# Kernel optimization log

Hardware: AMD Instinct MI355X
Metric: run time of the kernel (lower is better)

Reference implementation:

```python
import jax, jax.numpy as jnp
import numpy as np

DIM = 768
HEADS = 12
HEAD_DIM = DIM // HEADS
HIDDEN = int(DIM * 4.0)
EPS = 1e-5


def _layernorm(x, g, b):
    mu = jnp.mean(x, axis=-1, keepdims=True)
    var = jnp.var(x, axis=-1, keepdims=True)
    return (x - mu) * jax.lax.rsqrt(var + EPS) * g + b


def setup_inputs() -> dict:
    key = jax.random.key(0)
    ks = jax.random.split(key, 12)
    s = 0.02
    return {
        "x": jax.random.normal(ks[0], (8, 1024, DIM), dtype=jnp.float32),
        "norm1_g": jnp.ones((DIM,), jnp.float32),
        "norm1_b": jnp.zeros((DIM,), jnp.float32),
        "qkv_w": jax.random.normal(ks[1], (3 * DIM, DIM), jnp.float32) * s,
        "qkv_b": jnp.zeros((3 * DIM,), jnp.float32),
        "proj_w": jax.random.normal(ks[2], (DIM, DIM), jnp.float32) * s,
        "proj_b": jnp.zeros((DIM,), jnp.float32),
        "norm2_g": jnp.ones((DIM,), jnp.float32),
        "norm2_b": jnp.zeros((DIM,), jnp.float32),
        "fc1_w": jax.random.normal(ks[3], (HIDDEN, DIM), jnp.float32) * s,
        "fc1_b": jnp.zeros((HIDDEN,), jnp.float32),
        "fc2_w": jax.random.normal(ks[4], (DIM, HIDDEN), jnp.float32) * s,
        "fc2_b": jnp.zeros((DIM,), jnp.float32),
    }


def reference(x, norm1_g, norm1_b, qkv_w, qkv_b, proj_w, proj_b,
              norm2_g, norm2_b, fc1_w, fc1_b, fc2_w, fc2_b):
    B, N, C = x.shape
    scale = HEAD_DIM ** -0.5

    # --- MHSA with pre-norm + residual ---
    h = _layernorm(x, norm1_g, norm1_b)
    qkv = h @ qkv_w.T + qkv_b                      # [B, N, 3C]
    qkv = qkv.reshape(B, N, 3, HEADS, HEAD_DIM)
    qkv = jnp.transpose(qkv, (2, 0, 3, 1, 4))      # [3, B, H, N, Dh]
    q, k, v = qkv[0], qkv[1], qkv[2]
    attn = jnp.einsum("bhnd,bhmd->bhnm", q, k) * scale
    attn = jax.nn.softmax(attn, axis=-1)
    o = jnp.einsum("bhnm,bhmd->bhnd", attn, v)     # [B, H, N, Dh]
    o = jnp.transpose(o, (0, 2, 1, 3)).reshape(B, N, C)
    x = x + (o @ proj_w.T + proj_b)

    # --- MLP with pre-norm + residual ---
    h = _layernorm(x, norm2_g, norm2_b)
    h = jax.nn.gelu(h @ fc1_w.T + fc1_b, approximate=False)
    x = x + (h @ fc2_w.T + fc2_b)
    return x
```

## Files before the change

### kernel.cpp

```cpp
#include <hip/hip_runtime.h>
#include <hip/hip_bf16.h>

typedef unsigned short u16;
using short8  = __attribute__((ext_vector_type(8))) short;
using floatx4 = __attribute__((ext_vector_type(4))) float;

__device__ inline u16 f2bu(float f) {
    __hip_bfloat16 h = __float2bfloat16(f);
    return __builtin_bit_cast(u16, h);
}
__device__ inline float b2f(u16 u) {
    unsigned v = (unsigned)u << 16;
    return __builtin_bit_cast(float, v);
}
__device__ inline float gelu_f(float v) {
    float u = 1.5957691216f * (v + 0.044715f * v * v * v);
    return v / (1.f + __expf(-u));
}

__device__ inline void load16(const u16* g, u16* l) {
    __builtin_amdgcn_global_load_lds(
        (const __attribute__((address_space(1))) void*)g,
        (__attribute__((address_space(3))) void*)l, 16, 0, 0);
}

__global__ void cvt_bf16v(const float4* __restrict__ in, ushort4* __restrict__ out, int n4) {
    int i = blockIdx.x * 256 + threadIdx.x;
    if (i < n4) {
        float4 f = in[i];
        ushort4 r;
        r.x = f2bu(f.x); r.y = f2bu(f.y); r.z = f2bu(f.z); r.w = f2bu(f.w);
        out[i] = r;
    }
}

__global__ __launch_bounds__(256) void layernorm_bf16(
    const float* __restrict__ x, const float* __restrict__ g,
    const float* __restrict__ b, u16* __restrict__ out)
{
    int row = blockIdx.x;
    int tid = threadIdx.x;
    const float* xr = x + (size_t)row * 768;
    float v0 = xr[tid], v1 = xr[tid + 256], v2 = xr[tid + 512];
    float s = v0 + v1 + v2;
    float ss = v0 * v0 + v1 * v1 + v2 * v2;
    for (int off = 1; off < 64; off <<= 1) {
        s  += __shfl_xor(s, off, 64);
        ss += __shfl_xor(ss, off, 64);
    }
    __shared__ float as[4], ass[4];
    int wave = tid >> 6, lane = tid & 63;
    if (lane == 0) { as[wave] = s; ass[wave] = ss; }
    __syncthreads();
    s  = as[0] + as[1] + as[2] + as[3];
    ss = ass[0] + ass[1] + ass[2] + ass[3];
    float mu  = s * (1.0f / 768.0f);
    float var = ss * (1.0f / 768.0f) - mu * mu;
    float rs  = rsqrtf(var + 1e-5f);
    u16* orow = out + (size_t)row * 768;
    orow[tid]       = f2bu((v0 - mu) * rs * g[tid]       + b[tid]);
    orow[tid + 256] = f2bu((v1 - mu) * rs * g[tid + 256] + b[tid + 256]);
    orow[tid + 512] = f2bu((v2 - mu) * rs * g[tid + 512] + b[tid + 512]);
}

__global__ __launch_bounds__(256) void red2(
    const ushort4* __restrict__ P0, const ushort4* __restrict__ P1,
    const float* __restrict__ bias, const float4* __restrict__ res,
    float4* __restrict__ out)
{
    int i = blockIdx.x * 256 + threadIdx.x;
    int col = (i % 192) * 4;
    ushort4 a = P0[i], b = P1[i];
    float4 o = res ? res[i] : out[i];
    o.x += bias[col + 0] + b2f(a.x) + b2f(b.x);
    o.y += bias[col + 1] + b2f(a.y) + b2f(b.y);
    o.z += bias[col + 2] + b2f(a.z) + b2f(b.z);
    o.w += bias[col + 3] + b2f(a.w) + b2f(b.w);
    out[i] = o;
}

__global__ __launch_bounds__(256) void gemm_k64(
    const u16* __restrict__ A, int lda,
    const u16* __restrict__ B, int ldb,
    int K,
    const float* __restrict__ bias,
    const float* __restrict__ res,
    float* __restrict__ outf, u16* __restrict__ outb,
    u16* __restrict__ parts, size_t pstride,
    int ldc, int act, int splits)
{
    __shared__ u16 lsa[128 * 64];
    __shared__ u16 lsb[128 * 64];

    int tid  = threadIdx.x;
    int wave = tid >> 6, lane = tid & 63;
    int quad = lane >> 4, l16 = lane & 15;
    int wrow = (wave >> 1) * 64;
    int wcol = (wave & 1) * 64;

    int gx = gridDim.x;
    int nblk = gx * gridDim.y;
    int flat = blockIdx.y * gx + blockIdx.x;
    int d = (flat & 7) * (nblk >> 3) + (flat >> 3);
    int m0 = (d / gx) * 128, n0 = (d % gx) * 128;

    int Kper = K / splits;
    int kbeg = blockIdx.z * Kper;

    floatx4 acc[4][4];
    for (int i = 0; i < 4; ++i)
        for (int j = 0; j < 4; ++j)
            acc[i][j] = (floatx4){0.f, 0.f, 0.f, 0.f};

    int rsub = lane >> 3;
    int gc   = (lane & 7) ^ rsub;
    const u16* gA[4];
    const u16* gB[4];
    #pragma unroll
    for (int j = 0; j < 4; ++j) {
        int r = (j * 4 + wave) * 8 + rsub;
        gA[j] = A + (size_t)(m0 + r) * lda + kbeg + gc * 8;
        gB[j] = B + (size_t)(n0 + r) * ldb + kbeg + gc * 8;
    }

    int xq0 = ((quad)     ^ (l16 & 7)) * 8;
    int xq1 = ((quad + 4) ^ (l16 & 7)) * 8;

    for (int k0 = 0; k0 < Kper; k0 += 64) {
        __syncthreads();
        #pragma unroll
        for (int j = 0; j < 4; ++j) {
            load16(gA[j], &lsa[(j * 4 + wave) * 512]);
            gA[j] += 64;
        }
        #pragma unroll
        for (int j = 0; j < 4; ++j) {
            load16(gB[j], &lsb[(j * 4 + wave) * 512]);
            gB[j] += 64;
        }
        __syncthreads();

        short8 af[4], bfr[4];
        #pragma unroll
        for (int rb = 0; rb < 4; ++rb) af[rb]  = *(short8*)&lsa[(wrow + rb * 16 + l16) * 64 + xq0];
        #pragma unroll
        for (int cb = 0; cb < 4; ++cb) bfr[cb] = *(short8*)&lsb[(wcol + cb * 16 + l16) * 64 + xq0];
        #pragma unroll
        for (int rb = 0; rb < 4; ++rb)
            #pragma unroll
            for (int cb = 0; cb < 4; ++cb)
                acc[rb][cb] = __builtin_amdgcn_mfma_f32_16x16x32_bf16(af[rb], bfr[cb], acc[rb][cb], 0, 0, 0);
        #pragma unroll
        for (int rb = 0; rb < 4; ++rb) af[rb]  = *(short8*)&lsa[(wrow + rb * 16 + l16) * 64 + xq1];
        #pragma unroll
        for (int cb = 0; cb < 4; ++cb) bfr[cb] = *(short8*)&lsb[(wcol + cb * 16 + l16) * 64 + xq1];
        #pragma unroll
        for (int rb = 0; rb < 4; ++rb)
            #pragma unroll
            for (int cb = 0; cb < 4; ++cb)
                acc[rb][cb] = __builtin_amdgcn_mfma_f32_16x16x32_bf16(af[rb], bfr[cb], acc[rb][cb], 0, 0, 0);
    }

    u16* pdst = (splits > 1) ? parts + (size_t)blockIdx.z * pstride : nullptr;
    #pragma unroll
    for (int rb = 0; rb < 4; ++rb)
        #pragma unroll
        for (int cb = 0; cb < 4; ++cb)
            #pragma unroll
            for (int r = 0; r < 4; ++r) {
                int row = m0 + wrow + rb * 16 + quad * 4 + r;
                int col = n0 + wcol + cb * 16 + l16;
                float v = acc[rb][cb][r];
                if (splits > 1) {
                    pdst[(size_t)row * ldc + col] = f2bu(v);
                } else {
                    v += bias[col];
                    if (res) v += res[(size_t)row * ldc + col];
                    if (act) v = gelu_f(v);
                    if (outf) outf[(size_t)row * ldc + col] = v;
                    else      outb[(size_t)row * ldc + col] = f2bu(v);
                }
            }
}

__global__ __launch_bounds__(256) void attn_fused(
    const u16* __restrict__ qkv, u16* __restrict__ o)
{
    const int N = 1024, C3 = 2304;
    int qb = blockIdx.x;
    int bh = blockIdx.y;
    int b = bh / 12, h = bh % 12;
    int tid = threadIdx.x, wave = tid >> 6, lane = tid & 63;
    int quad = lane >> 4, l16 = lane & 15;

    __shared__ u16 lk[64 * 64];
    __shared__ u16 lvt[64][72];
    __shared__ u16 lp[4][16][72];

    const size_t base = (size_t)b * N * C3;
    int q0 = qb * 64 + wave * 16;

    short8 qa0 = *(const short8*)&qkv[base + (size_t)(q0 + l16) * C3 + h * 64 + quad * 8];
    short8 qa1 = *(const short8*)&qkv[base + (size_t)(q0 + l16) * C3 + h * 64 + 32 + quad * 8];

    floatx4 oacc[4];
    for (int i = 0; i < 4; ++i) oacc[i] = (floatx4){0.f, 0.f, 0.f, 0.f};
    float lsum[4] = {0.f, 0.f, 0.f, 0.f};

    for (int kt = 0; kt < N; kt += 64) {
        __syncthreads();
        #pragma unroll
        for (int i = 0; i < 2; ++i) {
            int idx = i * 2048 + wave * 512 + lane * 8;
            int r = idx >> 6;
            int gc = (lane & 7) ^ (r & 7);
            load16(&qkv[base + (size_t)(kt + r) * C3 + 768 + h * 64 + gc * 8], &lk[idx]);
        }
        {
            int key = tid & 63, dbase = (tid >> 6) * 16;
            const u16* vp = &qkv[base + (size_t)(kt + key) * C3 + 1536 + h * 64 + dbase];
            uint4 vv0 = *(const uint4*)vp;
            uint4 vv1 = *(const uint4*)(vp + 8);
            const u16* e0 = (const u16*)&vv0;
            const u16* e1 = (const u16*)&vv1;
            #pragma unroll
            for (int i = 0; i < 8; ++i) {
                lvt[dbase + i][key]     = e0[i];
                lvt[dbase + 8 + i][key] = e1[i];
            }
        }
        __syncthreads();

        float p[4][4];
        #pragma unroll
        for (int kb = 0; kb < 4; ++kb) {
            int R = kb * 16 + l16;
            short8 b0 = *(short8*)&lk[R * 64 + ((quad ^ (R & 7)) * 8)];
            short8 b1 = *(short8*)&lk[R * 64 + (((quad + 4) ^ (R & 7)) * 8)];
            floatx4 c = (floatx4){0.f, 0.f, 0.f, 0.f};
            c = __builtin_amdgcn_mfma_f32_16x16x32_bf16(qa0, b0, c, 0, 0, 0);
            c = __builtin_amdgcn_mfma_f32_16x16x32_bf16(qa1, b1, c, 0, 0, 0);
            #pragma unroll
            for (int r = 0; r < 4; ++r) {
                p[kb][r] = __expf(c[r] * 0.125f);
                lsum[r] += p[kb][r];
            }
        }
        #pragma unroll
        for (int kb = 0; kb < 4; ++kb)
            #pragma unroll
            for (int r = 0; r < 4; ++r)
                lp[wave][quad * 4 + r][kb * 16 + l16] = f2bu(p[kb][r]);

        short8 pa0 = *(short8*)&lp[wave][l16][quad * 8];
        short8 pa1 = *(short8*)&lp[wave][l16][32 + quad * 8];
        #pragma unroll
        for (int db = 0; db < 4; ++db) {
            short8 vb0 = *(short8*)&lvt[db * 16 + l16][quad * 8];
            short8 vb1 = *(short8*)&lvt[db * 16 + l16][32 + quad * 8];
            oacc[db] = __builtin_amdgcn_mfma_f32_16x16x32_bf16(pa0, vb0, oacc[db], 0, 0, 0);
            oacc[db] = __builtin_amdgcn_mfma_f32_16x16x32_bf16(pa1, vb1, oacc[db], 0, 0, 0);
        }
    }

    #pragma unroll
    for (int r = 0; r < 4; ++r)
        for (int off = 1; off < 16; off <<= 1)
            lsum[r] += __shfl_xor(lsum[r], off, 64);

    #pragma unroll
    for (int db = 0; db < 4; ++db)
        #pragma unroll
        for (int r = 0; r < 4; ++r) {
            int row = q0 + quad * 4 + r;
            int col = h * 64 + db * 16 + l16;
            o[(size_t)(b * N + row) * 768 + col] = f2bu(oacc[db][r] / lsum[r]);
        }
}

extern "C" void kernel_launch(void* const* d_in, const int* in_sizes, int n_in,
                              void* d_out, int out_size, void* d_ws, size_t ws_size,
                              hipStream_t stream) {
    const float* x      = (const float*)d_in[0];
    const float* n1g    = (const float*)d_in[1];
    const float* n1b    = (const float*)d_in[2];
    const float* qkv_w  = (const float*)d_in[3];
    const float* qkv_b  = (const float*)d_in[4];
    const float* proj_w = (const float*)d_in[5];
    const float* proj_b = (const float*)d_in[6];
    const float* n2g    = (const float*)d_in[7];
    const float* n2b    = (const float*)d_in[8];
    const float* fc1_w  = (const float*)d_in[9];
    const float* fc1_b  = (const float*)d_in[10];
    const float* fc2_w  = (const float*)d_in[11];
    const float* fc2_b  = (const float*)d_in[12];
    float* out = (float*)d_out;

    const int T = 8192;
    char* ws = (char*)d_ws;
    u16* w_qkv  = (u16*)ws;               ws += (size_t)2304 * 768 * 2;
    u16* w_proj = (u16*)ws;               ws += (size_t)768 * 768 * 2;
    u16* w_fc1  = (u16*)ws;               ws += (size_t)3072 * 768 * 2;
    u16* w_fc2  = (u16*)ws;               ws += (size_t)768 * 3072 * 2;
    u16* h_buf  = (u16*)ws;               ws += (size_t)T * 768 * 2;
    u16* qkvbuf = (u16*)ws;               ws += (size_t)T * 2304 * 2;
    u16* o_buf  = (u16*)ws;               ws += (size_t)T * 768 * 2;
    u16* pbuf   = (u16*)ws;               ws += (size_t)T * 768 * 2;
    u16* fc1out = qkvbuf;
    bool do_split = (size_t)(ws - (char*)d_ws) <= ws_size;
    size_t pstr = (size_t)(pbuf - h_buf);

    cvt_bf16v<<<dim3(2304 * 768 / 4 / 256), 256, 0, stream>>>((const float4*)qkv_w,  (ushort4*)w_qkv,  2304 * 768 / 4);
    cvt_bf16v<<<dim3(768 * 768 / 4 / 256),  256, 0, stream>>>((const float4*)proj_w, (ushort4*)w_proj, 768 * 768 / 4);
    cvt_bf16v<<<dim3(3072 * 768 / 4 / 256), 256, 0, stream>>>((const float4*)fc1_w,  (ushort4*)w_fc1,  3072 * 768 / 4);
    cvt_bf16v<<<dim3(768 * 3072 / 4 / 256), 256, 0, stream>>>((const float4*)fc2_w,  (ushort4*)w_fc2,  768 * 3072 / 4);

    layernorm_bf16<<<dim3(T), 256, 0, stream>>>(x, n1g, n1b, h_buf);
    gemm_k64<<<dim3(2304 / 128, T / 128), 256, 0, stream>>>(
        h_buf, 768, w_qkv, 768, 768, qkv_b, nullptr, nullptr, qkvbuf, nullptr, 0, 2304, 0, 1);
    attn_fused<<<dim3(16, 96), 256, 0, stream>>>(qkvbuf, o_buf);
    if (do_split) {
        gemm_k64<<<dim3(768 / 128, T / 128, 2), 256, 0, stream>>>(
            o_buf, 768, w_proj, 768, 768, proj_b, nullptr, nullptr, nullptr,
            h_buf, pstr, 768, 0, 2);
        red2<<<dim3(T * 768 / 4 / 256), 256, 0, stream>>>(
            (const ushort4*)h_buf, (const ushort4*)pbuf, proj_b, (const float4*)x, (float4*)out);
    } else {
        gemm_k64<<<dim3(768 / 128, T / 128), 256, 0, stream>>>(
            o_buf, 768, w_proj, 768, 768, proj_b, x, out, nullptr, nullptr, 0, 768, 0, 1);
    }
    layernorm_bf16<<<dim3(T), 256, 0, stream>>>(out, n2g, n2b, h_buf);
    gemm_k64<<<dim3(3072 / 128, T / 128), 256, 0, stream>>>(
        h_buf, 768, w_fc1, 768, 768, fc1_b, nullptr, nullptr, fc1out, nullptr, 0, 3072, 1, 1);
    if (do_split) {
        gemm_k64<<<dim3(768 / 128, T / 128, 2), 256, 0, stream>>>(
            fc1out, 3072, w_fc2, 3072, 3072, fc2_b, nullptr, nullptr, nullptr,
            h_buf, pstr, 768, 0, 2);
        red2<<<dim3(T * 768 / 4 / 256), 256, 0, stream>>>(
            (const ushort4*)h_buf, (const ushort4*)pbuf, fc2_b, nullptr, (float4*)out);
    } else {
        gemm_k64<<<dim3(768 / 128, T / 128), 256, 0, stream>>>(
            fc1out, 3072, w_fc2, 3072, 3072, fc2_b, out, out, nullptr, nullptr, 0, 768, 0, 1);
    }
}
```

Before: 418.4 us.

## Fuse split-K reduction with LayerNorm2 and double query rows per attention wave

Replaces the proj split-K reduction plus separate LayerNorm with a single row-wise kernel that sums the partials, adds the residual, writes the output and emits the normalized bf16 activations. This drops one full pass over the activation tensor. The attention kernel now gives each wave 32 query rows instead of 16, so every K/V tile loaded into LDS is reused across twice the queries, at the cost of more registers and half as many blocks. The fused kernel reads the partials from h_buf and writes the normalized output back into h_buf. This is safe only because each element is read before its own thread overwrites it.

```diff
diff --git a/kernel.cpp b/kernel.cpp
--- a/kernel.cpp
+++ b/kernel.cpp
@@ -79,6 +79,47 @@
     out[i] = o;
 }
 
+__global__ __launch_bounds__(256) void red2_ln(
+    const u16* __restrict__ P0, const u16* __restrict__ P1,
+    const float* __restrict__ bias, const float* __restrict__ x,
+    float* __restrict__ out,
+    const float* __restrict__ g, const float* __restrict__ bb,
+    u16* __restrict__ h)
+{
+    int row = blockIdx.x;
+    int tid = threadIdx.x;
+    size_t base = (size_t)row * 768;
+    float v[3];
+    float s = 0.f, ss = 0.f;
+    #pragma unroll
+    for (int j = 0; j < 3; ++j) {
+        int col = tid + j * 256;
+        size_t idx = base + col;
+        float o = x[idx] + bias[col] + b2f(P0[idx]) + b2f(P1[idx]);
+        out[idx] = o;
+        v[j] = o;
+        s += o; ss += o * o;
+    }
+    for (int off = 1; off < 64; off <<= 1) {
+        s  += __shfl_xor(s, off, 64);
+        ss += __shfl_xor(ss, off, 64);
+    }
+    __shared__ float as[4], ass[4];
+    int wave = tid >> 6, lane = tid & 63;
+    if (lane == 0) { as[wave] = s; ass[wave] = ss; }
+    __syncthreads();
+    s  = as[0] + as[1] + as[2] + as[3];
+    ss = ass[0] + ass[1] + ass[2] + ass[3];
+    float mu  = s * (1.0f / 768.0f);
+    float var = ss * (1.0f / 768.0f) - mu * mu;
+    float rs  = rsqrtf(var + 1e-5f);
+    #pragma unroll
+    for (int j = 0; j < 3; ++j) {
+        int col = tid + j * 256;
+        h[base + col] = f2bu((v[j] - mu) * rs * g[col] + bb[col]);
+    }
+}
+
 __global__ __launch_bounds__(256) void gemm_k64(
     const u16* __restrict__ A, int lda,
     const u16* __restrict__ B, int ldb,
@@ -195,17 +236,24 @@
 
     __shared__ u16 lk[64 * 64];
     __shared__ u16 lvt[64][72];
-    __shared__ u16 lp[4][16][72];
+    __shared__ u16 lp[4][32][72];
 
     const size_t base = (size_t)b * N * C3;
-    int q0 = qb * 64 + wave * 16;
-
-    short8 qa0 = *(const short8*)&qkv[base + (size_t)(q0 + l16) * C3 + h * 64 + quad * 8];
-    short8 qa1 = *(const short8*)&qkv[base + (size_t)(q0 + l16) * C3 + h * 64 + 32 + quad * 8];
-
-    floatx4 oacc[4];
-    for (int i = 0; i < 4; ++i) oacc[i] = (floatx4){0.f, 0.f, 0.f, 0.f};
-    float lsum[4] = {0.f, 0.f, 0.f, 0.f};
+    int q0 = qb * 128 + wave * 32;
+
+    short8 qa[2][2];
+    #pragma unroll
+    for (int rb = 0; rb < 2; ++rb)
+        #pragma unroll
+        for (int ch = 0; ch < 2; ++ch)
+            qa[rb][ch] = *(const short8*)&qkv[base + (size_t)(q0 + rb * 16 + l16) * C3 + h * 64 + ch * 32 + quad * 8];
+
+    floatx4 oacc[2][4];
+    #pragma unroll
+    for (int i = 0; i < 2; ++i)
+        #pragma unroll
+        for (int j = 0; j < 4; ++j) oacc[i][j] = (floatx4){0.f, 0.f, 0.f, 0.f};
+    float lsum[2][4] = {};
 
     for (int kt = 0; kt < N; kt += 64) {
         __syncthreads();
@@ -231,51 +279,60 @@
         }
         __syncthreads();
 
-        float p[4][4];
         #pragma unroll
         for (int kb = 0; kb < 4; ++kb) {
             int R = kb * 16 + l16;
             short8 b0 = *(short8*)&lk[R * 64 + ((quad ^ (R & 7)) * 8)];
             short8 b1 = *(short8*)&lk[R * 64 + (((quad + 4) ^ (R & 7)) * 8)];
-            floatx4 c = (floatx4){0.f, 0.f, 0.f, 0.f};
-            c = __builtin_amdgcn_mfma_f32_16x16x32_bf16(qa0, b0, c, 0, 0, 0);
-            c = __builtin_amdgcn_mfma_f32_16x16x32_bf16(qa1, b1, c, 0, 0, 0);
-            #pragma unroll
-            for (int r = 0; r < 4; ++r) {
-                p[kb][r] = __expf(c[r] * 0.125f);
-                lsum[r] += p[kb][r];
+            #pragma unroll
+            for (int rb = 0; rb < 2; ++rb) {
+                floatx4 c = (floatx4){0.f, 0.f, 0.f, 0.f};
+                c = __builtin_amdgcn_mfma_f32_16x16x32_bf16(qa[rb][0], b0, c, 0, 0, 0);
+                c = __builtin_amdgcn_mfma_f32_16x16x32_bf16(qa[rb][1], b1, c, 0, 0, 0);
+                #pragma unroll
+                for (int r = 0; r < 4; ++r) {
+                    float p = __expf(c[r] * 0.125f);
+                    lsum[rb][r] += p;
+                    lp[wave][rb * 16 + quad * 4 + r][kb * 16 + l16] = f2bu(p);
+                }
             }
         }
-        #pragma unroll
-        for (int kb = 0; kb < 4; ++kb)
-            #pragma unroll
-            for (int r = 0; r < 4; ++r)
-                lp[wave][quad * 4 + r][kb * 16 + l16] = f2bu(p[kb][r]);
-
-        short8 pa0 = *(short8*)&lp[wave][l16][quad * 8];
-        short8 pa1 = *(short8*)&lp[wave][l16][32 + quad * 8];
+
+        short8 pa[2][2];
+        #pragma unroll
+        for (int rb = 0; rb < 2; ++rb) {
+            pa[rb][0] = *(short8*)&lp[wave][rb * 16 + l16][quad * 8];
+            pa[rb][1] = *(short8*)&lp[wave][rb * 16 + l16][32 + quad * 8];
+        }
         #pragma unroll
         for (int db = 0; db < 4; ++db) {
             short8 vb0 = *(short8*)&lvt[db * 16 + l16][quad * 8];
             short8 vb1 = *(short8*)&lvt[db * 16 + l16][32 + quad * 8];
-            oacc[db] = __builtin_amdgcn_mfma_f32_16x16x32_bf16(pa0, vb0, oacc[db], 0, 0, 0);
-            oacc[db] = __builtin_amdgcn_mfma_f32_16x16x32_bf16(pa1, vb1, oacc[db], 0, 0, 0);
-        }
-    }
-
-    #pragma unroll
-    for (int r = 0; r < 4; ++r)
-        for (int off = 1; off < 16; off <<= 1)
-            lsum[r] += __shfl_xor(lsum[r], off, 64);
-
-    #pragma unroll
-    for (int db = 0; db < 4; ++db)
-        #pragma unroll
-        for (int r = 0; r < 4; ++r) {
-            int row = q0 + quad * 4 + r;
-            int col = h * 64 + db * 16 + l16;
-            o[(size_t)(b * N + row) * 768 + col] = f2bu(oacc[db][r] / lsum[r]);
-        }
+            #pragma unroll
+            for (int rb = 0; rb < 2; ++rb) {
+                oacc[rb][db] = __builtin_amdgcn_mfma_f32_16x16x32_bf16(pa[rb][0], vb0, oacc[rb][db], 0, 0, 0);
+                oacc[rb][db] = __builtin_amdgcn_mfma_f32_16x16x32_bf16(pa[rb][1], vb1, oacc[rb][db], 0, 0, 0);
+            }
+        }
+    }
+
+    #pragma unroll
+    for (int rb = 0; rb < 2; ++rb)
+        #pragma unroll
+        for (int r = 0; r < 4; ++r)
+            for (int off = 1; off < 16; off <<= 1)
+                lsum[rb][r] += __shfl_xor(lsum[rb][r], off, 64);
+
+    #pragma unroll
+    for (int rb = 0; rb < 2; ++rb)
+        #pragma unroll
+        for (int db = 0; db < 4; ++db)
+            #pragma unroll
+            for (int r = 0; r < 4; ++r) {
+                int row = q0 + rb * 16 + quad * 4 + r;
+                int col = h * 64 + db * 16 + l16;
+                o[(size_t)(b * N + row) * 768 + col] = f2bu(oacc[rb][db][r] / lsum[rb][r]);
+            }
 }
 
 extern "C" void kernel_launch(void* const* d_in, const int* in_sizes, int n_in,
@@ -318,18 +375,18 @@
     layernorm_bf16<<<dim3(T), 256, 0, stream>>>(x, n1g, n1b, h_buf);
     gemm_k64<<<dim3(2304 / 128, T / 128), 256, 0, stream>>>(
         h_buf, 768, w_qkv, 768, 768, qkv_b, nullptr, nullptr, qkvbuf, nullptr, 0, 2304, 0, 1);
-    attn_fused<<<dim3(16, 96), 256, 0, stream>>>(qkvbuf, o_buf);
+    attn_fused<<<dim3(8, 96), 256, 0, stream>>>(qkvbuf, o_buf);
     if (do_split) {
         gemm_k64<<<dim3(768 / 128, T / 128, 2), 256, 0, stream>>>(
             o_buf, 768, w_proj, 768, 768, proj_b, nullptr, nullptr, nullptr,
             h_buf, pstr, 768, 0, 2);
-        red2<<<dim3(T * 768 / 4 / 256), 256, 0, stream>>>(
-            (const ushort4*)h_buf, (const ushort4*)pbuf, proj_b, (const float4*)x, (float4*)out);
+        red2_ln<<<dim3(T), 256, 0, stream>>>(
+            h_buf, pbuf, proj_b, x, out, n2g, n2b, h_buf);
     } else {
         gemm_k64<<<dim3(768 / 128, T / 128), 256, 0, stream>>>(
             o_buf, 768, w_proj, 768, 768, proj_b, x, out, nullptr, nullptr, 0, 768, 0, 1);
-    }
-    layernorm_bf16<<<dim3(T), 256, 0, stream>>>(out, n2g, n2b, h_buf);
+        layernorm_bf16<<<dim3(T), 256, 0, stream>>>(out, n2g, n2b, h_buf);
+    }
     gemm_k64<<<dim3(3072 / 128, T / 128), 256, 0, stream>>>(
         h_buf, 768, w_fc1, 768, 768, fc1_b, nullptr, nullptr, fc1out, nullptr, 0, 3072, 1, 1);
     if (do_split) {
```

Measured after the change: 405.4 us. 1.03x faster.
